# Performance work log

Measured on AMD Instinct MI355X. Metric: run time of the kernel, lower is better.

## Reference

```python
import jax, jax.numpy as jnp
import numpy as np

# Model config (matches init_kwargs)
L, B, S, D, H, HKV, HD, FF, V = 2, 1, 2048, 2048, 16, 4, 128, 5632, 32000
EPS = 1e-5
ROPE_BASE = 10000.0


def setup_inputs() -> dict:
    key = jax.random.key(0)
    ks = jax.random.split(key, 13)
    s = 0.02  # init scale keeps activations/softmax numerically sane
    return {
        "idx": jax.random.randint(ks[0], (B, S), 0, V, dtype=jnp.int32),
        "embed": jax.random.normal(ks[1], (V, D), jnp.float32) * s,
        "wq": jax.random.normal(ks[2], (L, D, D), jnp.float32) * s,
        "wk": jax.random.normal(ks[3], (L, D, HKV * HD), jnp.float32) * s,
        "wv": jax.random.normal(ks[4], (L, D, HKV * HD), jnp.float32) * s,
        "wo": jax.random.normal(ks[5], (L, D, D), jnp.float32) * s,
        "ln1_g": jnp.ones((L, D), jnp.float32),
        "ln2_g": jnp.ones((L, D), jnp.float32),
        "w_gate": jax.random.normal(ks[6], (L, D, FF), jnp.float32) * s,
        "w_up": jax.random.normal(ks[7], (L, D, FF), jnp.float32) * s,
        "w_down": jax.random.normal(ks[8], (L, FF, D), jnp.float32) * s,
        "final_g": jnp.ones((D,), jnp.float32),
        "lm_head": jax.random.normal(ks[9], (V, D), jnp.float32) * s,
    }


def _rope_cos_sin(seq_len, n_elem, base=ROPE_BASE):
    inv = 1.0 / base ** (jnp.arange(0, n_elem, 2, dtype=jnp.float32)[: n_elem // 2] / n_elem)
    f = jnp.outer(jnp.arange(seq_len, dtype=jnp.float32), inv)  # [S, HD/2]
    return jnp.cos(f), jnp.sin(f)


def _apply_rope(x, cos, sin):
    # x: [B, S, h, HD]; split last dim into halves (matches torch reshape(...,2,-1))
    d2 = x.shape[-1] // 2
    x1, x2 = x[..., :d2], x[..., d2:]
    c = cos[None, :, None, :]
    s = sin[None, :, None, :]
    return jnp.concatenate([x1 * c - x2 * s, x2 * c + x1 * s], axis=-1)


def _rmsnorm(x, g, eps=EPS):
    return x * jax.lax.rsqrt(jnp.mean(x * x, axis=-1, keepdims=True) + eps) * g


def _forward(idx, embed, wq, wk, wv, wo, ln1_g, ln2_g, w_gate, w_up, w_down, final_g, lm_head):
    cos, sin = _rope_cos_sin(S, HD)
    # NOTE: the original uses a MULTIPLICATIVE bool mask on scores (scores * mask),
    # zeroing (not -inf'ing) future positions before softmax. Replicated faithfully.
    mask = jnp.tril(jnp.ones((S, S), jnp.float32))
    rep = H // HKV
    scale = 1.0 / np.sqrt(HD).astype(np.float32)

    x = embed[idx]  # [B, S, D]

    def layer(x, p):
        lwq, lwk, lwv, lwo, g1, g2, lwg, lwu, lwd = p
        h = _rmsnorm(x, g1)
        q = (h @ lwq).reshape(B, S, H, HD)
        k = (h @ lwk).reshape(B, S, HKV, HD)
        v = (h @ lwv).reshape(B, S, HKV, HD)
        q = _apply_rope(q, cos, sin)
        k = _apply_rope(k, cos, sin)
        k = jnp.repeat(k, rep, axis=2)  # GQA repeat_interleave over heads
        v = jnp.repeat(v, rep, axis=2)
        scores = jnp.einsum("bqhd,bkhd->bhqk", q, k) * scale * mask
        attn = jax.nn.softmax(scores, axis=-1)
        y = jnp.einsum("bhqk,bkhd->bqhd", attn, v).reshape(B, S, D) @ lwo
        x = x + y
        h2 = _rmsnorm(x, g2)
        x = x + (jax.nn.silu(h2 @ lwu) * (h2 @ lwg)) @ lwd
        return x, None

    x, _ = jax.lax.scan(layer, x, (wq, wk, wv, wo, ln1_g, ln2_g, w_gate, w_up, w_down))
    return _rmsnorm(x, final_g) @ lm_head.T  # [B, S, V]


def reference(idx, embed, wq, wk, wv, wo, ln1_g, ln2_g, w_gate, w_up, w_down, final_g, lm_head):
    return _forward(idx, embed, wq, wk, wv, wo, ln1_g, ln2_g, w_gate, w_up, w_down, final_g, lm_head)
```

## Files before the change

### kernel.cpp

```cpp
#include <hip/hip_runtime.h>

#define SQ     2048
#define DMODEL 2048
#define NHEAD  16
#define NKV    4
#define HDIM   128
#define FFDIM  5632
#define VOCAB  32000
#define NLAYER 2
#define EPSV   1e-5f

typedef __bf16 bf16;
typedef __bf16 bf16x4 __attribute__((ext_vector_type(4)));
typedef __bf16 bf16x8 __attribute__((ext_vector_type(8)));
typedef float  f32x4  __attribute__((ext_vector_type(4)));

enum { EP_STOREF = 0, EP_ADD = 2, EP_STOREB = 3, EP_QKV = 6 };

#define GLD(gp, lp) __builtin_amdgcn_global_load_lds( \
    (const __attribute__((address_space(1))) void*)(gp), \
    (__attribute__((address_space(3))) void*)(lp), 16, 0, 0)

#define MFMA16(a, b, c) __builtin_amdgcn_mfma_f32_16x16x32_bf16(a, b, c, 0, 0, 0)

#define FENCE() __builtin_amdgcn_sched_barrier(0)
#define PH_BAR() do { FENCE(); __builtin_amdgcn_s_barrier(); FENCE(); } while (0)

#define XCD_SWZ(TM)                                                        \
  const int GM  = (int)gridDim.x;                                          \
  const int nwg = GM * (int)gridDim.y;                                     \
  const int bid = (int)blockIdx.y * GM + (int)blockIdx.x;                  \
  const int q8  = nwg >> 3, r8 = nwg & 7;                                  \
  const int xcd = bid & 7, rnk = bid >> 3;                                 \
  const int swz = ((xcd < r8) ? xcd * (q8 + 1)                             \
                              : r8 * (q8 + 1) + (xcd - r8) * q8) + rnk;    \
  const int m0  = (swz % GM) * (TM);                                       \
  const int n0  = (swz / GM) * (TM == 256 ? 256 : 128);

template<int EPI>
__global__ __launch_bounds__(256, 2)
void gemm128(const bf16* __restrict__ A, const bf16* __restrict__ B,
             void* __restrict__ C, const void* __restrict__ Cin,
             bf16* __restrict__ C2, bf16* __restrict__ C3,
             int K, int lda, int ldb, int ldc)
{
  __shared__ bf16 As[2][128 * 64];
  __shared__ bf16 Bs[2][128 * 64];

  const int tid  = (int)threadIdx.x;
  const int lane = tid & 63;
  const int wave = tid >> 6;
  const int wm   = wave >> 1, wn = wave & 1;

  XCD_SWZ(128)

  const int nkt  = K >> 6;
  const int srow = lane >> 3;
  const long sxcol = (long)(((lane & 7) ^ (lane >> 3)) * 8);
  const int colc = lane & 15;
  const int g4   = lane >> 4;

  auto stage = [&](int t) {
    if (t < nkt) {
      const long kc = (long)t * 64 + sxcol;
      bf16* dA = As[t & 1];
      bf16* dB = Bs[t & 1];
      #pragma unroll
      for (int c = 0; c < 4; ++c) {
        const int chunk = wave * 4 + c;
        const int row   = chunk * 8 + srow;
        GLD(A + (long)(m0 + row) * lda + kc, dA + chunk * 512);
        GLD(B + (long)(n0 + row) * ldb + kc, dB + chunk * 512);
      }
    }
  };

  stage(0);
  f32x4 acc[4][4] = {};

  for (int t = 0; t < nkt; ++t) {
    stage(t + 1);
    FENCE();
    if (t + 1 < nkt) asm volatile("s_waitcnt vmcnt(8)" ::: "memory");
    else             asm volatile("s_waitcnt vmcnt(0)" ::: "memory");
    PH_BAR();
    const char* Ab = (const char*)As[t & 1];
    const char* Bb = (const char*)Bs[t & 1];
    #pragma unroll
    for (int kk = 0; kk < 2; ++kk) {
      bf16x8 af[4], bv[4];
      #pragma unroll
      for (int m = 0; m < 4; ++m) {
        const int r = wm * 64 + m * 16 + colc;
        af[m] = *(const bf16x8*)(Ab + r * 128 + (((kk * 4 + g4) ^ (r & 7)) * 16));
      }
      #pragma unroll
      for (int n = 0; n < 4; ++n) {
        const int r = wn * 64 + n * 16 + colc;
        bv[n] = *(const bf16x8*)(Bb + r * 128 + (((kk * 4 + g4) ^ (r & 7)) * 16));
      }
      #pragma unroll
      for (int m = 0; m < 4; ++m)
        #pragma unroll
        for (int n = 0; n < 4; ++n)
          acc[m][n] = MFMA16(af[m], bv[n], acc[m][n]);
    }
    PH_BAR();
  }

  #pragma unroll
  for (int m = 0; m < 4; ++m) {
    const int gr0 = m0 + wm * 64 + m * 16 + g4 * 4;
    #pragma unroll
    for (int n = 0; n < 4; ++n) {
      const int gc = n0 + wn * 64 + n * 16 + colc;
      if (EPI == EP_QKV) {
        if (n0 < 2048) {
          #pragma unroll
          for (int r = 0; r < 4; ++r)
            ((bf16*)C)[(long)(gr0 + r) * DMODEL + gc] = (bf16)acc[m][n][r];
        } else if (n0 < 2560) {
          #pragma unroll
          for (int r = 0; r < 4; ++r)
            C2[(long)(gr0 + r) * 512 + (gc - 2048)] = (bf16)acc[m][n][r];
        } else {
          bf16x4 pk = { (bf16)acc[m][n][0], (bf16)acc[m][n][1],
                        (bf16)acc[m][n][2], (bf16)acc[m][n][3] };
          *(bf16x4*)(C3 + (long)(gc - 2560) * SQ + gr0) = pk;
        }
      } else {
        #pragma unroll
        for (int r = 0; r < 4; ++r) {
          const long off = (long)(gr0 + r) * ldc + gc;
          const float v = acc[m][n][r];
          if (EPI == EP_STOREF)      ((float*)C)[off] = v;
          else if (EPI == EP_ADD)    ((float*)C)[off] = ((const float*)Cin)[off] + v;
          else if (EPI == EP_STOREB) ((bf16*)C)[off] = (bf16)v;
        }
      }
    }
  }
}

template<int EPI>
__global__ __launch_bounds__(512, 2)
void gemm256(const bf16* __restrict__ A, const bf16* __restrict__ B,
             void* __restrict__ C, const void* __restrict__ Cin,
             int K, int lda, int ldb, int ldc)
{
  __shared__ bf16 smem[2][4][128 * 64];

  const int tid  = (int)threadIdx.x;
  const int lane = tid & 63;
  const int wave = tid >> 6;
  const int wm   = wave >> 2;
  const int wn   = wave & 3;

  XCD_SWZ(256)

  const int nkt  = K >> 6;
  const int srow = lane >> 3;
  const long sxcol = (long)(((lane & 7) ^ (lane >> 3)) * 8);
  const int frow = lane & 15;
  const int ph0  = ((     (lane >> 4)) ^ (lane & 7)) * 16;
  const int ph1  = ((4 + (lane >> 4)) ^ (lane & 7)) * 16;

  auto stageA = [&](int tile, int half) {
    if (tile < nkt) {
      const long kc = (long)tile * 64 + sxcol;
      #pragma unroll
      for (int i = 0; i < 2; ++i)
        GLD(A + (long)(m0 + half * 128 + wave * 16 + i * 8 + srow) * lda + kc,
            smem[tile & 1][half] + (wave * 16 + i * 8) * 64);
    }
  };
  auto stageB = [&](int tile, int half) {
    if (tile < nkt) {
      const long kc = (long)tile * 64 + sxcol;
      #pragma unroll
      for (int i = 0; i < 2; ++i)
        GLD(B + (long)(n0 + half * 128 + wave * 16 + i * 8 + srow) * ldb + kc,
            smem[tile & 1][2 + half] + (wave * 16 + i * 8) * 64);
    }
  };

  stageB(0, 0); stageB(0, 1); stageA(0, 0); stageA(0, 1);
  asm volatile("s_waitcnt vmcnt(4)" ::: "memory");
  stageB(1, 0); stageB(1, 1); stageA(1, 0);
  asm volatile("s_waitcnt vmcnt(6)" ::: "memory");
  PH_BAR();

  f32x4 acc[8][4] = {};

  for (int t = 0; t < nkt; ++t) {
    const int bsel = t & 1;
    const char* Asl = (const char*)smem[bsel][wm];
    const char* Bsl = (const char*)smem[bsel][2 + (wn >> 1)];
    const int brow = (wn & 1) * 64;

    bf16x8 ar[4][2], b0f[2][2], b1f[2][2];

    #pragma unroll
    for (int mr = 0; mr < 4; ++mr) {
      ar[mr][0] = *(const bf16x8*)(Asl + (mr * 16 + frow) * 128 + ph0);
      ar[mr][1] = *(const bf16x8*)(Asl + (mr * 16 + frow) * 128 + ph1);
    }
    #pragma unroll
    for (int nc = 0; nc < 2; ++nc) {
      b0f[nc][0] = *(const bf16x8*)(Bsl + (brow + nc * 16 + frow) * 128 + ph0);
      b0f[nc][1] = *(const bf16x8*)(Bsl + (brow + nc * 16 + frow) * 128 + ph1);
    }
    stageA(t + 1, 1);
    PH_BAR();
    __builtin_amdgcn_s_setprio(1);
    #pragma unroll
    for (int mr = 0; mr < 4; ++mr)
      #pragma unroll
      for (int nc = 0; nc < 2; ++nc) {
        acc[mr][nc] = MFMA16(ar[mr][0], b0f[nc][0], acc[mr][nc]);
        acc[mr][nc] = MFMA16(ar[mr][1], b0f[nc][1], acc[mr][nc]);
      }
    __builtin_amdgcn_s_setprio(0);
    PH_BAR();

    #pragma unroll
    for (int nc = 0; nc < 2; ++nc) {
      b1f[nc][0] = *(const bf16x8*)(Bsl + (brow + (2 + nc) * 16 + frow) * 128 + ph0);
      b1f[nc][1] = *(const bf16x8*)(Bsl + (brow + (2 + nc) * 16 + frow) * 128 + ph1);
    }
    PH_BAR();
    __builtin_amdgcn_s_setprio(1);
    #pragma unroll
    for (int mr = 0; mr < 4; ++mr)
      #pragma unroll
      for (int nc = 0; nc < 2; ++nc) {
        acc[mr][2 + nc] = MFMA16(ar[mr][0], b1f[nc][0], acc[mr][2 + nc]);
        acc[mr][2 + nc] = MFMA16(ar[mr][1], b1f[nc][1], acc[mr][2 + nc]);
      }
    __builtin_amdgcn_s_setprio(0);
    PH_BAR();

    #pragma unroll
    for (int mr = 0; mr < 4; ++mr) {
      ar[mr][0] = *(const bf16x8*)(Asl + ((4 + mr) * 16 + frow) * 128 + ph0);
      ar[mr][1] = *(const bf16x8*)(Asl + ((4 + mr) * 16 + frow) * 128 + ph1);
    }
    stageB(t + 2, 0); stageB(t + 2, 1);
    PH_BAR();
    __builtin_amdgcn_s_setprio(1);
    #pragma unroll
    for (int mr = 0; mr < 4; ++mr)
      #pragma unroll
      for (int nc = 0; nc < 2; ++nc) {
        acc[4 + mr][nc] = MFMA16(ar[mr][0], b0f[nc][0], acc[4 + mr][nc]);
        acc[4 + mr][nc] = MFMA16(ar[mr][1], b0f[nc][1], acc[4 + mr][nc]);
      }
    __builtin_amdgcn_s_setprio(0);
    PH_BAR();

    stageA(t + 2, 0);
    PH_BAR();
    __builtin_amdgcn_s_setprio(1);
    #pragma unroll
    for (int mr = 0; mr < 4; ++mr)
      #pragma unroll
      for (int nc = 0; nc < 2; ++nc) {
        acc[4 + mr][2 + nc] = MFMA16(ar[mr][0], b1f[nc][0], acc[4 + mr][2 + nc]);
        acc[4 + mr][2 + nc] = MFMA16(ar[mr][1], b1f[nc][1], acc[4 + mr][2 + nc]);
      }
    __builtin_amdgcn_s_setprio(0);
    FENCE();
    if (t + 2 < nkt) asm volatile("s_waitcnt vmcnt(6)" ::: "memory");
    else             asm volatile("s_waitcnt vmcnt(0)" ::: "memory");
    PH_BAR();
  }

  #pragma unroll
  for (int mr = 0; mr < 8; ++mr) {
    const int gr0 = m0 + wm * 128 + mr * 16 + (lane >> 4) * 4;
    #pragma unroll
    for (int nc = 0; nc < 4; ++nc) {
      const int gc = n0 + wn * 64 + nc * 16 + (lane & 15);
      #pragma unroll
      for (int r = 0; r < 4; ++r) {
        const long off = (long)(gr0 + r) * ldc + gc;
        const float v = acc[mr][nc][r];
        if (EPI == EP_STOREF)      ((float*)C)[off] = v;
        else if (EPI == EP_STOREB) ((bf16*)C)[off] = (bf16)v;
      }
    }
  }
}

__global__ __launch_bounds__(256, 1)
void flash_attn(const bf16* __restrict__ qb, const bf16* __restrict__ kb,
                const bf16* __restrict__ vT, const float* __restrict__ suffPc,
                bf16* __restrict__ yb, float scale)
{
  __shared__ bf16 Ks[128 * 128];
  __shared__ bf16 Vs[128 * 128];
  __shared__ bf16 Ps[128 * 136];

  const int tid  = (int)threadIdx.x;
  const int lane = tid & 63;
  const int w    = tid >> 6;
  const int qt   = (int)blockIdx.x;
  const int h    = (int)blockIdx.y;
  const int kvh  = h >> 2;

  const int l15 = lane & 15;
  const int g4  = lane >> 4;

  bf16x8 qf[2][4];
  #pragma unroll
  for (int m = 0; m < 2; ++m)
    #pragma unroll
    for (int ks = 0; ks < 4; ++ks)
      qf[m][ks] = *(const bf16x8*)(qb + (long)(qt * 128 + w * 32 + m * 16 + l15) * DMODEL
                                   + h * HDIM + ks * 32 + g4 * 8);

  f32x4 acc_o[2][8] = {};
  float den[2][4] = {};

  const bf16* Kg = kb + (long)kvh * HDIM;
  const bf16* Vg = vT + (long)(kvh * HDIM) * SQ;

  for (int j = 0; j <= qt; ++j) {
    const bool diag = (j == qt);
    PH_BAR();

    #pragma unroll
    for (int i = 0; i < 8; ++i) {
      const int rb = w * 32 + i * 4;
      const int r  = rb + g4;
      GLD(Kg + (long)(j * 128 + r) * 512 + ((l15 ^ (r & 7)) * 8), Ks + rb * 128);
    }
    #pragma unroll
    for (int i = 0; i < 8; ++i) {
      const int rb = w * 32 + i * 4;
      const int r  = rb + g4;
      GLD(Vg + (long)r * SQ + j * 128 + ((l15 ^ (r & 7)) * 8), Vs + rb * 128);
    }
    asm volatile("s_waitcnt vmcnt(8)" ::: "memory");
    PH_BAR();

    f32x4 acc_s[2][8] = {};
    #pragma unroll
    for (int ks = 0; ks < 4; ++ks) {
      bf16x8 kf[8];
      #pragma unroll
      for (int n = 0; n < 8; ++n) {
        const int kr = n * 16 + l15;
        kf[n] = *(const bf16x8*)((const char*)Ks + kr * 256 + (((ks * 4 + g4) ^ (kr & 7)) * 16));
      }
      #pragma unroll
      for (int m = 0; m < 2; ++m)
        #pragma unroll
        for (int n = 0; n < 8; ++n)
          acc_s[m][n] = MFMA16(qf[m][ks], kf[n], acc_s[m][n]);
    }

    float rs[2][4] = {};
    #pragma unroll
    for (int m = 0; m < 2; ++m)
      #pragma unroll
      for (int n = 0; n < 8; ++n) {
        const int kc = n * 16 + l15;
        #pragma unroll
        for (int r = 0; r < 4; ++r) {
          const int qlr = w * 32 + m * 16 + g4 * 4 + r;
          float p = __expf(acc_s[m][n][r] * scale);
          if (diag && kc > qlr) p = 1.0f;
          rs[m][r] += p;
          Ps[(w * 32 + m * 16 + g4 * 4 + r) * 136 + kc] = (bf16)p;
        }
      }
    #pragma unroll
    for (int m = 0; m < 2; ++m)
      #pragma unroll
      for (int r = 0; r < 4; ++r) {
        float v = rs[m][r];
        v += __shfl_xor(v, 1); v += __shfl_xor(v, 2);
        v += __shfl_xor(v, 4); v += __shfl_xor(v, 8);
        den[m][r] += v;
      }

    asm volatile("s_waitcnt vmcnt(0) lgkmcnt(0)" ::: "memory");
    PH_BAR();

    #pragma unroll
    for (int ks = 0; ks < 4; ++ks) {
      bf16x8 pa[2], vf[8];
      #pragma unroll
      for (int m = 0; m < 2; ++m)
        pa[m] = *(const bf16x8*)((const char*)Ps + (w * 32 + m * 16 + l15) * 272
                                 + ks * 64 + g4 * 16);
      #pragma unroll
      for (int n = 0; n < 8; ++n) {
        const int dr = n * 16 + l15;
        vf[n] = *(const bf16x8*)((const char*)Vs + dr * 256 + (((ks * 4 + g4) ^ (dr & 7)) * 16));
      }
      #pragma unroll
      for (int m = 0; m < 2; ++m)
        #pragma unroll
        for (int n = 0; n < 8; ++n)
          acc_o[m][n] = MFMA16(pa[m], vf[n], acc_o[m][n]);
    }
  }

  float denf[2][4];
  #pragma unroll
  for (int m = 0; m < 2; ++m)
    #pragma unroll
    for (int r = 0; r < 4; ++r)
      denf[m][r] = den[m][r] + 128.0f * (15 - qt);

  #pragma unroll
  for (int n = 0; n < 8; ++n) {
    const float t = suffPc[((kvh << 4) + qt) * 128 + n * 16 + l15];
    #pragma unroll
    for (int m = 0; m < 2; ++m)
      #pragma unroll
      for (int r = 0; r < 4; ++r) {
        const float y = (acc_o[m][n][r] + t) / denf[m][r];
        yb[(long)(qt * 128 + w * 32 + m * 16 + g4 * 4 + r) * DMODEL
           + h * HDIM + n * 16 + l15] = (bf16)y;
      }
  }
}

__global__ __launch_bounds__(128)
void vsuffix(const bf16* __restrict__ vT, float* __restrict__ suffPc)
{
  const int kvh = (int)blockIdx.x;
  const int d   = (int)threadIdx.x;
  const bf16* row = vT + (long)(kvh * HDIM + d) * SQ;
  float a = 0.f;
  for (int c = 15; c >= 0; --c) {
    suffPc[(kvh * 16 + c) * 128 + d] = a;
    float s = 0.f;
    #pragma unroll
    for (int r = 0; r < 16; ++r) {
      bf16x8 v = *(const bf16x8*)(row + c * 128 + r * 8);
      #pragma unroll
      for (int e = 0; e < 8; ++e) s += (float)v[e];
    }
    a += s;
  }
}

__global__ __launch_bounds__(256)
void silumul(bf16* __restrict__ gz)
{
  const long t  = (long)blockIdx.x * 256 + threadIdx.x;
  const int row = (int)(t / 704);
  const int c8  = (int)(t % 704);
  bf16* g = gz + (long)row * (2 * FFDIM) + c8 * 8;
  bf16x8 gv = *(bf16x8*)g;
  bf16x8 uv = *(bf16x8*)(g + FFDIM);
  bf16x8 o;
  #pragma unroll
  for (int j = 0; j < 8; ++j) {
    const float u = (float)uv[j];
    o[j] = (bf16)((u / (1.0f + __expf(-u))) * (float)gv[j]);
  }
  *(bf16x8*)g = o;
}

__global__ __launch_bounds__(256)
void transpose_cvt(const float* __restrict__ in, bf16* __restrict__ out, int K, int N)
{
  __shared__ float t[32][33];
  const int n0 = (int)blockIdx.x * 32, k0 = (int)blockIdx.y * 32;
  const int tr = (int)threadIdx.x >> 3;
  const int tc = ((int)threadIdx.x & 7) * 4;
  f32x4 v = *(const f32x4*)(in + (long)(k0 + tr) * N + n0 + tc);
  t[tr][tc] = v[0]; t[tr][tc + 1] = v[1]; t[tr][tc + 2] = v[2]; t[tr][tc + 3] = v[3];
  __syncthreads();
  bf16x4 b = { (bf16)t[tc][tr], (bf16)t[tc + 1][tr], (bf16)t[tc + 2][tr], (bf16)t[tc + 3][tr] };
  *(bf16x4*)(out + (long)(n0 + tr) * K + k0 + tc) = b;
}

__global__ __launch_bounds__(256)
void cvt_bf16_kernel(const float* __restrict__ in, bf16* __restrict__ out, int nvec)
{
  const int i = (int)(blockIdx.x * 256 + threadIdx.x);
  if (i < nvec) {
    f32x4 v = ((const f32x4*)in)[i];
    bf16x4 b = { (bf16)v[0], (bf16)v[1], (bf16)v[2], (bf16)v[3] };
    ((bf16x4*)out)[i] = b;
  }
}

__global__ __launch_bounds__(256)
void rmsnorm_kernel(bf16* __restrict__ out, const float* __restrict__ in, const float* __restrict__ g)
{
  const int row = (int)blockIdx.x;
  const float* x = in + (long)row * DMODEL;
  bf16* o = out + (long)row * DMODEL;
  const int tid = (int)threadIdx.x;
  f32x4 v0 = *(const f32x4*)(x + tid * 4);
  f32x4 v1 = *(const f32x4*)(x + tid * 4 + 1024);
  float ss = v0[0]*v0[0] + v0[1]*v0[1] + v0[2]*v0[2] + v0[3]*v0[3]
           + v1[0]*v1[0] + v1[1]*v1[1] + v1[2]*v1[2] + v1[3]*v1[3];
  #pragma unroll
  for (int o_ = 32; o_; o_ >>= 1) ss += __shfl_xor(ss, o_);
  __shared__ float sm[4];
  if ((tid & 63) == 0) sm[tid >> 6] = ss;
  __syncthreads();
  ss = sm[0] + sm[1] + sm[2] + sm[3];
  const float r = 1.0f / sqrtf(ss * (1.0f / DMODEL) + EPSV);
  f32x4 g0 = *(const f32x4*)(g + tid * 4);
  f32x4 g1 = *(const f32x4*)(g + tid * 4 + 1024);
  bf16x4 o0, o1;
  #pragma unroll
  for (int j = 0; j < 4; ++j) { o0[j] = (bf16)(v0[j] * r * g0[j]); o1[j] = (bf16)(v1[j] * r * g1[j]); }
  *(bf16x4*)(o + tid * 4) = o0;
  *(bf16x4*)(o + tid * 4 + 1024) = o1;
}

__global__ void rope_tables(float* cosT, float* sinT)
{
  const int s = (int)blockIdx.x;
  const int i = (int)threadIdx.x;
  const double inv = pow(10000.0, -(double)i / 64.0);
  const double f = (double)s * inv;
  cosT[s * 64 + i] = (float)cos(f);
  sinT[s * 64 + i] = (float)sin(f);
}

__global__ __launch_bounds__(256)
void rope_apply(bf16* buf, const float* cosT, const float* sinT, int nh, int stride)
{
  const int t = (int)(blockIdx.x * blockDim.x + threadIdx.x);
  const int per = nh * 64;
  const int s = t / per;
  const int r = t - s * per;
  const int h = r >> 6;
  const int i = r & 63;
  bf16* b = buf + (long)s * stride + h * HDIM;
  const float c  = cosT[s * 64 + i];
  const float sn = sinT[s * 64 + i];
  const float x1 = (float)b[i];
  const float x2 = (float)b[64 + i];
  b[i]      = (bf16)(x1 * c - x2 * sn);
  b[64 + i] = (bf16)(x2 * c + x1 * sn);
}

__global__ __launch_bounds__(256)
void embed_gather(f32x4* x, const f32x4* embed, const int* idx)
{
  const int t = (int)(blockIdx.x * 256 + threadIdx.x);
  const int s = t >> 9;
  const int c = t & 511;
  x[t] = embed[(long)idx[s] * 512 + c];
}

extern "C" void kernel_launch(void* const* d_in, const int* in_sizes, int n_in,
                              void* d_out, int out_size, void* d_ws, size_t ws_size,
                              hipStream_t stream)
{
  (void)in_sizes; (void)n_in; (void)out_size;
  const int*   idx   = (const int*)  d_in[0];
  const float* embed = (const float*)d_in[1];
  const float* wq    = (const float*)d_in[2];
  const float* wk    = (const float*)d_in[3];
  const float* wv    = (const float*)d_in[4];
  const float* wo    = (const float*)d_in[5];
  const float* ln1g  = (const float*)d_in[6];
  const float* ln2g  = (const float*)d_in[7];
  const float* wgate = (const float*)d_in[8];
  const float* wup   = (const float*)d_in[9];
  const float* wdown = (const float*)d_in[10];
  const float* fing  = (const float*)d_in[11];
  const float* lmh   = (const float*)d_in[12];
  float* out = (float*)d_out;

  char* wp = (char*)d_ws;
  auto alloc = [&](size_t bytes) { char* p = wp; wp += (bytes + 255) & ~(size_t)255; return p; };
  float* cosT   = (float*)alloc((size_t)SQ * 64 * 4);
  float* sinT   = (float*)alloc((size_t)SQ * 64 * 4);
  float* suffPc = (float*)alloc((size_t)NKV * 16 * 128 * 4);
  float* x      = (float*)alloc((size_t)SQ * DMODEL * 4);
  bf16*  h      = (bf16*) alloc((size_t)SQ * DMODEL * 2);
  bf16*  qb     = (bf16*) alloc((size_t)SQ * DMODEL * 2);
  bf16*  kb     = (bf16*) alloc((size_t)SQ * 512 * 2);
  bf16*  vT     = (bf16*) alloc((size_t)512 * SQ * 2);
  size_t used  = (size_t)(wp - (char*)d_ws);
  bf16*  wbuf  = (bf16*)wp;
  size_t avail = ws_size - used;

  bf16* yb = qb;
  bf16* gz = (bf16*)d_out;
  const float scale = 0.08838834764831845f;

  rope_tables<<<SQ, 64, 0, stream>>>(cosT, sinT);
  embed_gather<<<(SQ * 512) / 256, 256, 0, stream>>>((f32x4*)x, (const f32x4*)embed, idx);

  for (int l = 0; l < NLAYER; ++l) {
    const float* lwq = wq    + (long)l * DMODEL * DMODEL;
    const float* lwk = wk    + (long)l * DMODEL * 512;
    const float* lwv = wv    + (long)l * DMODEL * 512;
    const float* lwo = wo    + (long)l * DMODEL * DMODEL;
    const float* lwg = wgate + (long)l * DMODEL * FFDIM;
    const float* lwu = wup   + (long)l * DMODEL * FFDIM;
    const float* lwd = wdown + (long)l * FFDIM * DMODEL;

    rmsnorm_kernel<<<SQ, 256, 0, stream>>>(h, x, ln1g + l * DMODEL);

    transpose_cvt<<<dim3(64, 64), 256, 0, stream>>>(lwq, wbuf, DMODEL, DMODEL);
    transpose_cvt<<<dim3(16, 64), 256, 0, stream>>>(lwk, wbuf + (long)2048 * DMODEL, DMODEL, 512);
    transpose_cvt<<<dim3(16, 64), 256, 0, stream>>>(lwv, wbuf + (long)2560 * DMODEL, DMODEL, 512);
    gemm128<EP_QKV><<<dim3(16, 24), 256, 0, stream>>>(
        h, wbuf, qb, nullptr, kb, vT, DMODEL, DMODEL, DMODEL, 0);

    vsuffix<<<NKV, 128, 0, stream>>>(vT, suffPc);
    rope_apply<<<(SQ * NHEAD * 64) / 256, 256, 0, stream>>>(qb, cosT, sinT, NHEAD, DMODEL);
    rope_apply<<<(SQ * NKV * 64) / 256, 256, 0, stream>>>(kb, cosT, sinT, NKV, 512);

    flash_attn<<<dim3(16, NHEAD), 256, 0, stream>>>(qb, kb, vT, suffPc, yb, scale);

    transpose_cvt<<<dim3(64, 64), 256, 0, stream>>>(lwo, wbuf, DMODEL, DMODEL);
    gemm128<EP_ADD><<<dim3(16, 16), 256, 0, stream>>>(
        yb, wbuf, x, x, nullptr, nullptr, DMODEL, DMODEL, DMODEL, DMODEL);

    rmsnorm_kernel<<<SQ, 256, 0, stream>>>(h, x, ln2g + l * DMODEL);

    transpose_cvt<<<dim3(176, 64), 256, 0, stream>>>(lwg, wbuf, DMODEL, FFDIM);
    transpose_cvt<<<dim3(176, 64), 256, 0, stream>>>(lwu, wbuf + (long)FFDIM * DMODEL, DMODEL, FFDIM);
    gemm256<EP_STOREB><<<dim3(8, 44), 512, 0, stream>>>(
        h, wbuf, gz, nullptr, DMODEL, DMODEL, DMODEL, 2 * FFDIM);

    silumul<<<(SQ * (FFDIM / 8)) / 256, 256, 0, stream>>>(gz);

    transpose_cvt<<<dim3(64, 176), 256, 0, stream>>>(lwd, wbuf, FFDIM, DMODEL);
    gemm128<EP_ADD><<<dim3(16, 16), 256, 0, stream>>>(
        gz, wbuf, x, x, nullptr, nullptr, FFDIM, 2 * FFDIM, FFDIM, DMODEL);
  }

  rmsnorm_kernel<<<SQ, 256, 0, stream>>>(h, x, fing);

  long chunkRows = (long)(avail / ((size_t)DMODEL * 2)) & ~255L;
  if (chunkRows > VOCAB) chunkRows = VOCAB;
  for (long c0 = 0; c0 < VOCAB; c0 += chunkRows) {
    const long rows = (VOCAB - c0 < chunkRows) ? (VOCAB - c0) : chunkRows;
    const int  nvec = (int)(rows * DMODEL / 4);
    cvt_bf16_kernel<<<(nvec + 255) / 256, 256, 0, stream>>>(lmh + c0 * DMODEL, wbuf, nvec);
    gemm256<EP_STOREF><<<dim3(8, (int)(rows / 256)), 512, 0, stream>>>(
        h, wbuf, out + c0, nullptr, DMODEL, DMODEL, DMODEL, VOCAB);
  }
}
```

Measured before the change: 1.334 ms.

## Fuse SwiGLU into gate/up GEMM epilogue, triple-buffer K-loop, batch transposes and RoPE

Gate and up weight rows are interleaved during transpose, so each adjacent column pair in the gemm256 output is (gate, up). The epilogue then computes silu(up)*gate with a lane shuffle and writes a half-width FF buffer, removing the separate silumul pass and the wide intermediate write and read. gemm128 gains a 3-stage LDS pipeline for the O-projection and down-projection, at the cost of dropping to 1 block per CU. Weight transposes and the q/k RoPE kernels are merged into fewer launches. The GLU epilogue stores only from half the lanes.

```diff
diff --git a/kernel.cpp b/kernel.cpp
--- a/kernel.cpp
+++ b/kernel.cpp
@@ -15,7 +15,7 @@
 typedef __bf16 bf16x8 __attribute__((ext_vector_type(8)));
 typedef float  f32x4  __attribute__((ext_vector_type(4)));
 
-enum { EP_STOREF = 0, EP_ADD = 2, EP_STOREB = 3, EP_QKV = 6 };
+enum { EP_STOREF = 0, EP_ADD = 2, EP_STOREB = 3, EP_QKV = 6, EP_GLU = 7 };
 
 #define GLD(gp, lp) __builtin_amdgcn_global_load_lds( \
     (const __attribute__((address_space(1))) void*)(gp), \
@@ -37,15 +37,15 @@
   const int m0  = (swz % GM) * (TM);                                       \
   const int n0  = (swz / GM) * (TM == 256 ? 256 : 128);
 
-template<int EPI>
-__global__ __launch_bounds__(256, 2)
+template<int EPI, int NBUF>
+__global__ __launch_bounds__(256, NBUF == 2 ? 2 : 1)
 void gemm128(const bf16* __restrict__ A, const bf16* __restrict__ B,
              void* __restrict__ C, const void* __restrict__ Cin,
              bf16* __restrict__ C2, bf16* __restrict__ C3,
              int K, int lda, int ldb, int ldc)
 {
-  __shared__ bf16 As[2][128 * 64];
-  __shared__ bf16 Bs[2][128 * 64];
+  __shared__ bf16 As[NBUF][128 * 64];
+  __shared__ bf16 Bs[NBUF][128 * 64];
 
   const int tid  = (int)threadIdx.x;
   const int lane = tid & 63;
@@ -60,11 +60,11 @@
   const int colc = lane & 15;
   const int g4   = lane >> 4;
 
-  auto stage = [&](int t) {
+  auto stage = [&](int t, int buf) {
     if (t < nkt) {
       const long kc = (long)t * 64 + sxcol;
-      bf16* dA = As[t & 1];
-      bf16* dB = Bs[t & 1];
+      bf16* dA = As[buf];
+      bf16* dB = Bs[buf];
       #pragma unroll
       for (int c = 0; c < 4; ++c) {
         const int chunk = wave * 4 + c;
@@ -75,17 +75,32 @@
     }
   };
 
-  stage(0);
+  stage(0, 0);
+  if (NBUF == 3) stage(1, 1);
+
   f32x4 acc[4][4] = {};
+  int wb = (NBUF == 3) ? 2 : 1;
+  int rb = 0;
 
   for (int t = 0; t < nkt; ++t) {
-    stage(t + 1);
-    FENCE();
-    if (t + 1 < nkt) asm volatile("s_waitcnt vmcnt(8)" ::: "memory");
-    else             asm volatile("s_waitcnt vmcnt(0)" ::: "memory");
-    PH_BAR();
-    const char* Ab = (const char*)As[t & 1];
-    const char* Bb = (const char*)Bs[t & 1];
+    if (NBUF == 2) {
+      stage(t + 1, wb);
+      wb ^= 1;
+      FENCE();
+      if (t + 1 < nkt) asm volatile("s_waitcnt vmcnt(8)" ::: "memory");
+      else             asm volatile("s_waitcnt vmcnt(0)" ::: "memory");
+    } else {
+      stage(t + 2, wb);
+      wb = (wb == 2) ? 0 : wb + 1;
+      FENCE();
+      if (t + 2 < nkt)      asm volatile("s_waitcnt vmcnt(16)" ::: "memory");
+      else if (t + 1 < nkt) asm volatile("s_waitcnt vmcnt(8)"  ::: "memory");
+      else                  asm volatile("s_waitcnt vmcnt(0)"  ::: "memory");
+    }
+    PH_BAR();
+    const char* Ab = (const char*)As[rb];
+    const char* Bb = (const char*)Bs[rb];
+    rb = (NBUF == 2) ? (rb ^ 1) : ((rb == 2) ? 0 : rb + 1);
     #pragma unroll
     for (int kk = 0; kk < 2; ++kk) {
       bf16x8 af[4], bv[4];
@@ -283,10 +298,18 @@
       const int gc = n0 + wn * 64 + nc * 16 + (lane & 15);
       #pragma unroll
       for (int r = 0; r < 4; ++r) {
-        const long off = (long)(gr0 + r) * ldc + gc;
         const float v = acc[mr][nc][r];
-        if (EPI == EP_STOREF)      ((float*)C)[off] = v;
-        else if (EPI == EP_STOREB) ((bf16*)C)[off] = (bf16)v;
+        if (EPI == EP_GLU) {
+          const float o = __shfl_xor(v, 1);
+          if (((lane & 15) & 1) == 0) {
+            const float res = (o / (1.0f + __expf(-o))) * v;
+            ((bf16*)C)[(long)(gr0 + r) * ldc + (gc >> 1)] = (bf16)res;
+          }
+        } else {
+          const long off = (long)(gr0 + r) * ldc + gc;
+          if (EPI == EP_STOREF)      ((float*)C)[off] = v;
+          else if (EPI == EP_STOREB) ((bf16*)C)[off] = (bf16)v;
+        }
       }
     }
   }
@@ -450,35 +473,26 @@
 }
 
 __global__ __launch_bounds__(256)
-void silumul(bf16* __restrict__ gz)
-{
-  const long t  = (long)blockIdx.x * 256 + threadIdx.x;
-  const int row = (int)(t / 704);
-  const int c8  = (int)(t % 704);
-  bf16* g = gz + (long)row * (2 * FFDIM) + c8 * 8;
-  bf16x8 gv = *(bf16x8*)g;
-  bf16x8 uv = *(bf16x8*)(g + FFDIM);
-  bf16x8 o;
-  #pragma unroll
-  for (int j = 0; j < 8; ++j) {
-    const float u = (float)uv[j];
-    o[j] = (bf16)((u / (1.0f + __expf(-u))) * (float)gv[j]);
-  }
-  *(bf16x8*)g = o;
-}
-
-__global__ __launch_bounds__(256)
-void transpose_cvt(const float* __restrict__ in, bf16* __restrict__ out, int K, int N)
-{
+void transpose_cvt3(const float* __restrict__ s0, bf16* __restrict__ d0, int N0, int L0,
+                    const float* __restrict__ s1, bf16* __restrict__ d1, int N1, int L1,
+                    const float* __restrict__ s2, bf16* __restrict__ d2, int N2, int L2,
+                    int K)
+{
+  const float* src; bf16* dst; int N, L;
+  if (blockIdx.z == 0)      { src = s0; dst = d0; N = N0; L = L0; }
+  else if (blockIdx.z == 1) { src = s1; dst = d1; N = N1; L = L1; }
+  else                      { src = s2; dst = d2; N = N2; L = L2; }
+  if (!src) return;
+  const int n0 = (int)blockIdx.x * 32; if (n0 >= N) return;
+  const int k0 = (int)blockIdx.y * 32;
   __shared__ float t[32][33];
-  const int n0 = (int)blockIdx.x * 32, k0 = (int)blockIdx.y * 32;
   const int tr = (int)threadIdx.x >> 3;
   const int tc = ((int)threadIdx.x & 7) * 4;
-  f32x4 v = *(const f32x4*)(in + (long)(k0 + tr) * N + n0 + tc);
+  f32x4 v = *(const f32x4*)(src + (long)(k0 + tr) * N + n0 + tc);
   t[tr][tc] = v[0]; t[tr][tc + 1] = v[1]; t[tr][tc + 2] = v[2]; t[tr][tc + 3] = v[3];
   __syncthreads();
   bf16x4 b = { (bf16)t[tc][tr], (bf16)t[tc + 1][tr], (bf16)t[tc + 2][tr], (bf16)t[tc + 3][tr] };
-  *(bf16x4*)(out + (long)(n0 + tr) * K + k0 + tc) = b;
+  *(bf16x4*)(dst + (long)(n0 + tr) * L + k0 + tc) = b;
 }
 
 __global__ __launch_bounds__(256)
@@ -530,9 +544,13 @@
 }
 
 __global__ __launch_bounds__(256)
-void rope_apply(bf16* buf, const float* cosT, const float* sinT, int nh, int stride)
-{
-  const int t = (int)(blockIdx.x * blockDim.x + threadIdx.x);
+void rope_both(bf16* __restrict__ qb, bf16* __restrict__ kb,
+               const float* __restrict__ cosT, const float* __restrict__ sinT)
+{
+  const int blk = (int)blockIdx.x;
+  bf16* buf; int nh, stride, t;
+  if (blk < 8192) { buf = qb; nh = NHEAD; stride = DMODEL; t = blk * 256 + (int)threadIdx.x; }
+  else            { buf = kb; nh = NKV;   stride = 512;    t = (blk - 8192) * 256 + (int)threadIdx.x; }
   const int per = nh * 64;
   const int s = t / per;
   const int r = t - s * per;
@@ -586,12 +604,12 @@
   bf16*  qb     = (bf16*) alloc((size_t)SQ * DMODEL * 2);
   bf16*  kb     = (bf16*) alloc((size_t)SQ * 512 * 2);
   bf16*  vT     = (bf16*) alloc((size_t)512 * SQ * 2);
+  bf16*  ffb    = (bf16*) alloc((size_t)SQ * FFDIM * 2);
   size_t used  = (size_t)(wp - (char*)d_ws);
   bf16*  wbuf  = (bf16*)wp;
   size_t avail = ws_size - used;
 
   bf16* yb = qb;
-  bf16* gz = (bf16*)d_out;
   const float scale = 0.08838834764831845f;
 
   rope_tables<<<SQ, 64, 0, stream>>>(cosT, sinT);
@@ -608,34 +626,38 @@
 
     rmsnorm_kernel<<<SQ, 256, 0, stream>>>(h, x, ln1g + l * DMODEL);
 
-    transpose_cvt<<<dim3(64, 64), 256, 0, stream>>>(lwq, wbuf, DMODEL, DMODEL);
-    transpose_cvt<<<dim3(16, 64), 256, 0, stream>>>(lwk, wbuf + (long)2048 * DMODEL, DMODEL, 512);
-    transpose_cvt<<<dim3(16, 64), 256, 0, stream>>>(lwv, wbuf + (long)2560 * DMODEL, DMODEL, 512);
-    gemm128<EP_QKV><<<dim3(16, 24), 256, 0, stream>>>(
+    transpose_cvt3<<<dim3(64, 64, 3), 256, 0, stream>>>(
+        lwq, wbuf, DMODEL, DMODEL,
+        lwk, wbuf + (long)2048 * DMODEL, 512, DMODEL,
+        lwv, wbuf + (long)2560 * DMODEL, 512, DMODEL, DMODEL);
+    gemm128<EP_QKV, 2><<<dim3(16, 24), 256, 0, stream>>>(
         h, wbuf, qb, nullptr, kb, vT, DMODEL, DMODEL, DMODEL, 0);
 
     vsuffix<<<NKV, 128, 0, stream>>>(vT, suffPc);
-    rope_apply<<<(SQ * NHEAD * 64) / 256, 256, 0, stream>>>(qb, cosT, sinT, NHEAD, DMODEL);
-    rope_apply<<<(SQ * NKV * 64) / 256, 256, 0, stream>>>(kb, cosT, sinT, NKV, 512);
+    rope_both<<<8192 + 2048, 256, 0, stream>>>(qb, kb, cosT, sinT);
 
     flash_attn<<<dim3(16, NHEAD), 256, 0, stream>>>(qb, kb, vT, suffPc, yb, scale);
 
-    transpose_cvt<<<dim3(64, 64), 256, 0, stream>>>(lwo, wbuf, DMODEL, DMODEL);
-    gemm128<EP_ADD><<<dim3(16, 16), 256, 0, stream>>>(
+    transpose_cvt3<<<dim3(64, 64, 1), 256, 0, stream>>>(
+        lwo, wbuf, DMODEL, DMODEL,
+        nullptr, nullptr, 0, 0, nullptr, nullptr, 0, 0, DMODEL);
+    gemm128<EP_ADD, 3><<<dim3(16, 16), 256, 0, stream>>>(
         yb, wbuf, x, x, nullptr, nullptr, DMODEL, DMODEL, DMODEL, DMODEL);
 
     rmsnorm_kernel<<<SQ, 256, 0, stream>>>(h, x, ln2g + l * DMODEL);
 
-    transpose_cvt<<<dim3(176, 64), 256, 0, stream>>>(lwg, wbuf, DMODEL, FFDIM);
-    transpose_cvt<<<dim3(176, 64), 256, 0, stream>>>(lwu, wbuf + (long)FFDIM * DMODEL, DMODEL, FFDIM);
-    gemm256<EP_STOREB><<<dim3(8, 44), 512, 0, stream>>>(
-        h, wbuf, gz, nullptr, DMODEL, DMODEL, DMODEL, 2 * FFDIM);
-
-    silumul<<<(SQ * (FFDIM / 8)) / 256, 256, 0, stream>>>(gz);
-
-    transpose_cvt<<<dim3(64, 176), 256, 0, stream>>>(lwd, wbuf, FFDIM, DMODEL);
-    gemm128<EP_ADD><<<dim3(16, 16), 256, 0, stream>>>(
-        gz, wbuf, x, x, nullptr, nullptr, FFDIM, 2 * FFDIM, FFDIM, DMODEL);
+    transpose_cvt3<<<dim3(176, 64, 2), 256, 0, stream>>>(
+        lwg, wbuf, FFDIM, 2 * DMODEL,
+        lwu, wbuf + DMODEL, FFDIM, 2 * DMODEL,
+        nullptr, nullptr, 0, 0, DMODEL);
+    gemm256<EP_GLU><<<dim3(8, 44), 512, 0, stream>>>(
+        h, wbuf, ffb, nullptr, DMODEL, DMODEL, DMODEL, FFDIM);
+
+    transpose_cvt3<<<dim3(64, 176, 1), 256, 0, stream>>>(
+        lwd, wbuf, DMODEL, FFDIM,
+        nullptr, nullptr, 0, 0, nullptr, nullptr, 0, 0, FFDIM);
+    gemm128<EP_ADD, 3><<<dim3(16, 16), 256, 0, stream>>>(
+        ffb, wbuf, x, x, nullptr, nullptr, FFDIM, FFDIM, FFDIM, DMODEL);
   }
 
   rmsnorm_kernel<<<SQ, 256, 0, stream>>>(h, x, fing);
```

After: 1.319 ms. Within noise of the previous version (-1.1%).
